# Optimization experiments

Measured on AMD Instinct MI355X. Metric: run time of the kernel, lower is better.

Reference implementation:

```python
import jax, jax.numpy as jnp
import numpy as np

GROUP_SIZE = 16
MIN_SIGMA = 1e-4


def setup_inputs() -> dict:
    key = jax.random.key(0)
    k1, k2, k3 = jax.random.split(key, 3)
    B, N, M, F = 4, 8192, 4096, 64
    return {
        "point_cloud": jax.random.normal(k1, (B, 3, N), dtype=jnp.float32),
        "query_cloud": jax.random.normal(k2, (B, 3, M), dtype=jnp.float32),
        "point_features": jax.random.normal(k3, (B, F, N), dtype=jnp.float32),
        "temperature": jnp.asarray(1.0, dtype=jnp.float32),
    }


def reference(point_cloud, query_cloud, point_features, temperature):
    # point_cloud: (B,3,N), query_cloud: (B,3,M), point_features: (B,F,N)
    k = GROUP_SIZE
    # Pairwise squared distances (B, M, N): ||q||^2 + ||p||^2 - 2 q.p
    q_sq = jnp.sum(query_cloud ** 2, axis=1)              # (B, M)
    p_sq = jnp.sum(point_cloud ** 2, axis=1)              # (B, N)
    qp = jnp.einsum('bdm,bdn->bmn', query_cloud, point_cloud)
    d2 = q_sq[:, :, None] + p_sq[:, None, :] - 2.0 * qp   # (B, M, N)
    # k nearest neighbors per query
    _, idx = jax.lax.top_k(-d2, k)                         # (B, M, k)

    # Gather neighbor coords and features: (B, 3, M, k), (B, F, M, k)
    idx_b = idx[:, None, :, :]                             # (B,1,M,k)
    grouped_points = jnp.take_along_axis(
        point_cloud[:, :, None, :], jnp.broadcast_to(idx_b, (idx.shape[0], 3, idx.shape[1], k)), axis=3)
    grouped_features = jnp.take_along_axis(
        point_features[:, :, None, :],
        jnp.broadcast_to(idx_b, (idx.shape[0], point_features.shape[1], idx.shape[1], k)), axis=3)

    # Soft-projection weights
    sigma = jnp.maximum(temperature ** 2, jnp.asarray(MIN_SIGMA, dtype=temperature.dtype))
    deltas = grouped_points - query_cloud[:, :, :, None]   # (B,3,M,k)
    dist = jnp.sum(deltas ** 2, axis=1, keepdims=True) / sigma  # (B,1,M,k)
    weights = jax.nn.softmax(-dist, axis=3)                # (B,1,M,k)

    projected_points = jnp.sum(grouped_points * weights, axis=3)     # (B,3,M)
    propagated_features = jnp.sum(grouped_features * weights, axis=3)  # (B,F,M)
    return (projected_points, propagated_features)
```

## Files before the change

kernel.cpp:

```cpp
#include <hip/hip_runtime.h>


#define BB 4
#define NN 8192
#define MM 4096
#define FF 64
#define KK 16
#define CHUNK 2048
#define NCHUNK 4
#define QPW 4
#define QPB 32
#define SCAP 54
#define NTHR 1024
#define STG 33

__global__ __launch_bounds__(256) void transpose_feat(const float* __restrict__ pf,
                                                      float* __restrict__ pfT) {
    __shared__ float tile[64][65];
    const int b = blockIdx.y;
    const int n0 = blockIdx.x * 64;
    const int t = threadIdx.x;
    const int n = t & 63, fq = t >> 6;
#pragma unroll
    for (int i = 0; i < 16; ++i) {
        int f = fq * 16 + i;
        tile[f][n] = pf[(size_t)b * FF * NN + (size_t)f * NN + n0 + n];
    }
    __syncthreads();
    const int f2 = t & 63, nq = t >> 6;
#pragma unroll
    for (int i = 0; i < 16; ++i) {
        int nn2 = nq * 16 + i;
        pfT[(size_t)b * NN * FF + (size_t)(n0 + nn2) * FF + f2] = tile[f2][nn2];
    }
}

__device__ __forceinline__ unsigned mapf(float f) {
    unsigned u = __float_as_uint(f);
    return (u & 0x80000000u) ? ~u : (u | 0x80000000u);
}
__device__ __forceinline__ float unmapf(unsigned k) {
    return (k & 0x80000000u) ? __uint_as_float(k ^ 0x80000000u)
                             : __uint_as_float(~k);
}

#define STAGE(C)                                                            \
    do {                                                                    \
        if (t < CHUNK / 4) {                                                \
            int base_ = (C)*CHUNK + t * 4;                                  \
            float4 x4_ = *(const float4*)(pcb + base_);                     \
            float4 y4_ = *(const float4*)(pcb + NN + base_);                \
            float4 z4_ = *(const float4*)(pcb + 2 * NN + base_);            \
            *(float4*)(s_pts + t * 4) = x4_;                                \
            *(float4*)(s_pts + CHUNK + t * 4) = y4_;                        \
            *(float4*)(s_pts + 2 * CHUNK + t * 4) = z4_;                    \
            float4 p4_;                                                     \
            p4_.x = fmaf(x4_.x, x4_.x, fmaf(y4_.x, y4_.x, z4_.x * z4_.x));  \
            p4_.y = fmaf(x4_.y, x4_.y, fmaf(y4_.y, y4_.y, z4_.y * z4_.y));  \
            p4_.z = fmaf(x4_.z, x4_.z, fmaf(y4_.z, y4_.z, z4_.z * z4_.z));  \
            p4_.w = fmaf(x4_.w, x4_.w, fmaf(y4_.w, y4_.w, z4_.w * z4_.w));  \
            *(float4*)(s_pts + 3 * CHUNK + t * 4) = p4_;                    \
        }                                                                   \
    } while (0)

#define VAL(X, Y, Z, PS, Q) \
    fmaf((X), qx2[Q], fmaf((Y), qy2[Q], fmaf((Z), qz2[Q], (PS))))

#define PUSH(WQ, V, I)                                          \
    do {                                                        \
        int pos_ = atomicAdd(&s_cnt[WQ], 1);                    \
        if (pos_ < SCAP) {                                      \
            s_surv[((WQ)*SCAP + pos_) * 2] = (V);               \
            s_surv[((WQ)*SCAP + pos_) * 2 + 1] = __int_as_float(I); \
        }                                                       \
    } while (0)

__global__ __launch_bounds__(NTHR, 8) void soft_proj_kernel(
    const float* __restrict__ pc, const float* __restrict__ qc,
    const float* __restrict__ pf, const float* __restrict__ pfT,
    const float* __restrict__ temp, float* __restrict__ out, int useT) {
    __shared__ __align__(16) float s_pts[4 * CHUNK];
    __shared__ __align__(16) float s_surv[QPB * SCAP * 2];
    __shared__ int s_cnt[QPB];
    __shared__ int s_sel[QPB * KK];
    __shared__ float s_thr[2 * QPB];

    const int bid = blockIdx.x;
    const int b = bid >> 7;
    const int m0 = (bid & 127) * QPB;
    const int t = threadIdx.x;
    const int wave = t >> 6;
    const int lane = t & 63;
    const int pairIdx = wave & 7;
    const int half = wave >> 3;

    const float* pcb = pc + (size_t)b * 3 * NN;
    const float* qcb = qc + (size_t)b * 3 * MM;

    float qx2[QPW], qy2[QPW], qz2[QPW];
#pragma unroll
    for (int q = 0; q < QPW; ++q) {
        int m = m0 + pairIdx * QPW + q;
        qx2[q] = -2.0f * qcb[m];
        qy2[q] = -2.0f * qcb[MM + m];
        qz2[q] = -2.0f * qcb[2 * MM + m];
    }

    float mn[QPW];
#pragma unroll
    for (int q = 0; q < QPW; ++q) mn[q] = 3.0e38f;

    for (int c = 0; c < NCHUNK; ++c) {
        __syncthreads();
        STAGE(c);
        __syncthreads();
        const int ob = half * 1024 + lane * 4;
#pragma unroll
        for (int g = 0; g < 4; ++g) {
            int oo = ob + g * 256;
            float4 x4 = *(const float4*)(s_pts + oo);
            float4 y4 = *(const float4*)(s_pts + CHUNK + oo);
            float4 z4 = *(const float4*)(s_pts + 2 * CHUNK + oo);
            float4 p4 = *(const float4*)(s_pts + 3 * CHUNK + oo);
#pragma unroll
            for (int q = 0; q < QPW; ++q) {
                float v0 = VAL(x4.x, y4.x, z4.x, p4.x, q);
                float v1 = VAL(x4.y, y4.y, z4.y, p4.y, q);
                float v2 = VAL(x4.z, y4.z, z4.z, p4.z, q);
                float v3 = VAL(x4.w, y4.w, z4.w, p4.w, q);
                mn[q] = fminf(mn[q], fminf(fminf(v0, v1), fminf(v2, v3)));
            }
        }
    }

    float thrv[QPW];
#pragma unroll
    for (int q = 0; q < QPW; ++q) {
        unsigned key = mapf(mn[q]);
        unsigned res = 0u;
        for (int bb = 31; bb >= 16; --bb) {
            unsigned cand = res | (1u << bb);
            unsigned long long bal = __ballot(key < cand);
            int c2 = __popcll(bal);
            if (c2 < 8) res = cand;
        }
        thrv[q] = unmapf(res | 0xFFFFu);
    }
    if (lane == 0) {
#pragma unroll
        for (int q = 0; q < QPW; ++q)
            s_thr[half * QPB + pairIdx * QPW + q] = thrv[q];
    }
    if (t < QPB) s_cnt[t] = 0;
    __syncthreads();
#pragma unroll
    for (int q = 0; q < QPW; ++q)
        thrv[q] = fmaxf(s_thr[pairIdx * QPW + q], s_thr[QPB + pairIdx * QPW + q]);

    for (int c = 0; c < NCHUNK; ++c) {
        __syncthreads();
        STAGE(c);
        __syncthreads();
        const int ob = half * 1024 + lane * 4;
#pragma unroll
        for (int g = 0; g < 4; ++g) {
            int oo = ob + g * 256;
            float4 x4 = *(const float4*)(s_pts + oo);
            float4 y4 = *(const float4*)(s_pts + CHUNK + oo);
            float4 z4 = *(const float4*)(s_pts + 2 * CHUNK + oo);
            float4 p4 = *(const float4*)(s_pts + 3 * CHUNK + oo);
            int gi = c * CHUNK + oo;
#pragma unroll
            for (int q = 0; q < QPW; ++q) {
                float v0 = VAL(x4.x, y4.x, z4.x, p4.x, q);
                float v1 = VAL(x4.y, y4.y, z4.y, p4.y, q);
                float v2 = VAL(x4.z, y4.z, z4.z, p4.z, q);
                float v3 = VAL(x4.w, y4.w, z4.w, p4.w, q);
                float m01 = fminf(v0, v1);
                float m23 = fminf(v2, v3);
                if (fminf(m01, m23) <= thrv[q]) {
                    int wqq = pairIdx * QPW + q;
                    if (v0 <= thrv[q]) PUSH(wqq, v0, gi + 0);
                    if (v1 <= thrv[q]) PUSH(wqq, v1, gi + 1);
                    if (v2 <= thrv[q]) PUSH(wqq, v2, gi + 2);
                    if (v3 <= thrv[q]) PUSH(wqq, v3, gi + 3);
                }
            }
        }
    }
    __syncthreads();

#pragma unroll
    for (int qq = 0; qq < 2; ++qq) {
        int wq = wave * 2 + qq;
        int cnt = s_cnt[wq];
        cnt = __builtin_amdgcn_readfirstlane(cnt);
        if (cnt > SCAP) cnt = SCAP;
        bool valid = lane < cnt;
        float mv = 0.f;
        int mi = 0;
        if (valid) {
            mv = s_surv[(wq * SCAP + lane) * 2];
            mi = __float_as_int(s_surv[(wq * SCAP + lane) * 2 + 1]);
        }
        int rank = 0;
        for (int j = 0; j < cnt; ++j) {
            float vj = s_surv[(wq * SCAP + j) * 2];
            int ij = __float_as_int(s_surv[(wq * SCAP + j) * 2 + 1]);
            if (valid && (vj < mv || (vj == mv && ij < mi))) rank++;
        }
        if (valid && rank < KK) s_sel[wq * KK + rank] = mi;
    }
    __syncthreads();

    float* stage = s_surv;
    float tval = temp[0];
    float sigma = fmaxf(tval * tval, 1.0e-4f);
    float inv_sigma = 1.0f / sigma;
    const float* pfTb = pfT + (size_t)b * NN * FF;
    const float* pfb = pf + (size_t)b * FF * NN;

#pragma unroll
    for (int qq = 0; qq < 2; ++qq) {
        int wq = wave * 2 + qq;
        int m = m0 + wq;
        float qxe = qcb[m], qye = qcb[MM + m], qze = qcb[2 * MM + m];
        int ik[KK];
        float dk[KK];
#pragma unroll
        for (int k = 0; k < KK; ++k) {
            int ii = __builtin_amdgcn_readfirstlane(s_sel[wq * KK + k]);
            ik[k] = ii;
            float px = pcb[ii], py = pcb[NN + ii], pz = pcb[2 * NN + ii];
            float dx = px - qxe, dy = py - qye, dz = pz - qze;
            dk[k] = fmaf(dx, dx, fmaf(dy, dy, dz * dz));
        }
        float dmin = dk[0];
#pragma unroll
        for (int k = 1; k < KK; ++k) dmin = fminf(dmin, dk[k]);
        float ssum = 0.f, facc = 0.f, sx = 0.f, sy = 0.f, sz = 0.f;
#pragma unroll
        for (int k = 0; k < KK; ++k) {
            float e = __expf((dmin - dk[k]) * inv_sigma);
            ssum += e;
            float px = pcb[ik[k]], py = pcb[NN + ik[k]], pz = pcb[2 * NN + ik[k]];
            sx = fmaf(e, px, sx);
            sy = fmaf(e, py, sy);
            sz = fmaf(e, pz, sz);
            float fv = useT ? pfTb[(size_t)ik[k] * FF + lane]
                            : pfb[(size_t)lane * NN + ik[k]];
            facc = fmaf(e, fv, facc);
        }
        float rs = 1.0f / ssum;
        stage[lane * STG + wq] = facc * rs;
        if (lane == 0) {
            stage[(64) * STG + wq] = sx * rs;
            stage[(65) * STG + wq] = sy * rs;
            stage[(66) * STG + wq] = sz * rs;
        }
    }
    __syncthreads();

    const size_t featOff = (size_t)BB * 3 * MM;
    for (int j = t; j < 67 * QPB; j += NTHR) {
        int row = j >> 5, col = j & 31;
        float v = stage[row * STG + col];
        int m = m0 + col;
        if (row < 64)
            out[featOff + (size_t)b * FF * MM + (size_t)row * MM + m] = v;
        else
            out[(size_t)b * 3 * MM + (size_t)(row - 64) * MM + m] = v;
    }
}

extern "C" void kernel_launch(void* const* d_in, const int* in_sizes, int n_in,
                              void* d_out, int out_size, void* d_ws, size_t ws_size,
                              hipStream_t stream) {
    (void)in_sizes; (void)n_in; (void)out_size;
    const float* pc = (const float*)d_in[0];
    const float* qc = (const float*)d_in[1];
    const float* pf = (const float*)d_in[2];
    const float* temp = (const float*)d_in[3];
    float* out = (float*)d_out;
    float* pfT = (float*)d_ws;
    const size_t needT = (size_t)BB * NN * FF * sizeof(float);
    int useT = (ws_size >= needT && d_ws != nullptr) ? 1 : 0;

    if (useT) {
        hipLaunchKernelGGL(transpose_feat, dim3(NN / 64, BB), dim3(256), 0, stream,
                           pf, pfT);
    }
    hipLaunchKernelGGL(soft_proj_kernel, dim3((BB * MM) / QPB), dim3(NTHR), 0,
                       stream, pc, qc, pf, pfT, temp, out, useT);
}
```

Measured before the change: 119.5 us.

## Double-buffer point chunks with async global-to-LDS loads and precomputed norms

Point coordinates plus squared norms are precomputed into a 4-plane workspace buffer by the prep kernel. Both scan passes then stream half-size chunks through double-buffered LDS using global_load_lds DMA, so the next chunk loads while the current one is evaluated, and one barrier per chunk replaces two. The min reductions use v_min3 with two independent accumulators. In exchange it needs extra workspace and twice as many chunk iterations.

```diff
diff --git a/kernel.cpp b/kernel.cpp
--- a/kernel.cpp
+++ b/kernel.cpp
@@ -6,20 +6,47 @@
 #define MM 4096
 #define FF 64
 #define KK 16
-#define CHUNK 2048
-#define NCHUNK 4
+#define CHUNK 1024
+#define NCHUNK 8
 #define QPW 4
 #define QPB 32
 #define SCAP 54
 #define NTHR 1024
 #define STG 33
 
-__global__ __launch_bounds__(256) void transpose_feat(const float* __restrict__ pf,
-                                                      float* __restrict__ pfT) {
-    __shared__ float tile[64][65];
+__device__ __forceinline__ void gload_lds16(const float* g, float* l) {
+    __builtin_amdgcn_global_load_lds(
+        (const __attribute__((address_space(1))) void*)g,
+        (__attribute__((address_space(3))) void*)l, 16, 0, 0);
+}
+
+__device__ __forceinline__ float min3f(float a, float b, float c) {
+    float d;
+    asm("v_min3_f32 %0, %1, %2, %3" : "=v"(d) : "v"(a), "v"(b), "v"(c));
+    return d;
+}
+
+__global__ __launch_bounds__(256) void prep_kernel(const float* __restrict__ pf,
+                                                   float* __restrict__ pfT,
+                                                   const float* __restrict__ pc,
+                                                   float* __restrict__ pc4,
+                                                   int doT, int doPS) {
     const int b = blockIdx.y;
     const int n0 = blockIdx.x * 64;
     const int t = threadIdx.x;
+    if (doPS && t < 64) {
+        int n = n0 + t;
+        const float* s = pc + (size_t)b * 3 * NN;
+        float x = s[n], y = s[NN + n], z = s[2 * NN + n];
+        float ps = fmaf(x, x, fmaf(y, y, z * z));
+        float* d = pc4 + (size_t)b * 4 * NN;
+        d[n] = x;
+        d[NN + n] = y;
+        d[2 * NN + n] = z;
+        d[3 * NN + n] = ps;
+    }
+    if (!doT) return;
+    __shared__ float tile[64][65];
     const int n = t & 63, fq = t >> 6;
 #pragma unroll
     for (int i = 0; i < 16; ++i) {
@@ -44,22 +71,28 @@
                              : __uint_as_float(~k);
 }
 
-#define STAGE(C)                                                            \
+#define ISSUE(C, BUF)                                                       \
     do {                                                                    \
-        if (t < CHUNK / 4) {                                                \
+        if (usePS) {                                                        \
+            int pl_ = t >> 8;                                               \
+            int ii_ = (t & 255) * 4;                                        \
+            gload_lds16(pc4b + pl_ * NN + (C)*CHUNK + ii_,                  \
+                        s_pts + (BUF) * (4 * CHUNK) + pl_ * CHUNK + ii_);   \
+        } else if (t < 256) {                                               \
             int base_ = (C)*CHUNK + t * 4;                                  \
             float4 x4_ = *(const float4*)(pcb + base_);                     \
             float4 y4_ = *(const float4*)(pcb + NN + base_);                \
             float4 z4_ = *(const float4*)(pcb + 2 * NN + base_);            \
-            *(float4*)(s_pts + t * 4) = x4_;                                \
-            *(float4*)(s_pts + CHUNK + t * 4) = y4_;                        \
-            *(float4*)(s_pts + 2 * CHUNK + t * 4) = z4_;                    \
+            float* bp_ = s_pts + (BUF) * (4 * CHUNK);                       \
+            *(float4*)(bp_ + t * 4) = x4_;                                  \
+            *(float4*)(bp_ + CHUNK + t * 4) = y4_;                          \
+            *(float4*)(bp_ + 2 * CHUNK + t * 4) = z4_;                      \
             float4 p4_;                                                     \
             p4_.x = fmaf(x4_.x, x4_.x, fmaf(y4_.x, y4_.x, z4_.x * z4_.x));  \
             p4_.y = fmaf(x4_.y, x4_.y, fmaf(y4_.y, y4_.y, z4_.y * z4_.y));  \
             p4_.z = fmaf(x4_.z, x4_.z, fmaf(y4_.z, y4_.z, z4_.z * z4_.z));  \
             p4_.w = fmaf(x4_.w, x4_.w, fmaf(y4_.w, y4_.w, z4_.w * z4_.w));  \
-            *(float4*)(s_pts + 3 * CHUNK + t * 4) = p4_;                    \
+            *(float4*)(bp_ + 3 * CHUNK + t * 4) = p4_;                      \
         }                                                                   \
     } while (0)
 
@@ -78,8 +111,9 @@
 __global__ __launch_bounds__(NTHR, 8) void soft_proj_kernel(
     const float* __restrict__ pc, const float* __restrict__ qc,
     const float* __restrict__ pf, const float* __restrict__ pfT,
-    const float* __restrict__ temp, float* __restrict__ out, int useT) {
-    __shared__ __align__(16) float s_pts[4 * CHUNK];
+    const float* __restrict__ pc4g, const float* __restrict__ temp,
+    float* __restrict__ out, int useT, int usePS) {
+    __shared__ __align__(16) float s_pts[2 * 4 * CHUNK];
     __shared__ __align__(16) float s_surv[QPB * SCAP * 2];
     __shared__ int s_cnt[QPB];
     __shared__ int s_sel[QPB * KK];
@@ -96,6 +130,7 @@
 
     const float* pcb = pc + (size_t)b * 3 * NN;
     const float* qcb = qc + (size_t)b * 3 * MM;
+    const float* pc4b = pc4g + (size_t)b * 4 * NN;
 
     float qx2[QPW], qy2[QPW], qz2[QPW];
 #pragma unroll
@@ -106,37 +141,40 @@
         qz2[q] = -2.0f * qcb[2 * MM + m];
     }
 
-    float mn[QPW];
-#pragma unroll
-    for (int q = 0; q < QPW; ++q) mn[q] = 3.0e38f;
-
+    float mnA[QPW], mnB[QPW];
+#pragma unroll
+    for (int q = 0; q < QPW; ++q) { mnA[q] = 3.0e38f; mnB[q] = 3.0e38f; }
+
+    ISSUE(0, 0);
+    __syncthreads();
     for (int c = 0; c < NCHUNK; ++c) {
-        __syncthreads();
-        STAGE(c);
-        __syncthreads();
-        const int ob = half * 1024 + lane * 4;
-#pragma unroll
-        for (int g = 0; g < 4; ++g) {
+        if (c + 1 < NCHUNK) ISSUE(c + 1, (c + 1) & 1);
+        const float* bp = s_pts + (c & 1) * (4 * CHUNK);
+        const int ob = half * 512 + lane * 4;
+#pragma unroll
+        for (int g = 0; g < 2; ++g) {
             int oo = ob + g * 256;
-            float4 x4 = *(const float4*)(s_pts + oo);
-            float4 y4 = *(const float4*)(s_pts + CHUNK + oo);
-            float4 z4 = *(const float4*)(s_pts + 2 * CHUNK + oo);
-            float4 p4 = *(const float4*)(s_pts + 3 * CHUNK + oo);
+            float4 x4 = *(const float4*)(bp + oo);
+            float4 y4 = *(const float4*)(bp + CHUNK + oo);
+            float4 z4 = *(const float4*)(bp + 2 * CHUNK + oo);
+            float4 p4 = *(const float4*)(bp + 3 * CHUNK + oo);
 #pragma unroll
             for (int q = 0; q < QPW; ++q) {
                 float v0 = VAL(x4.x, y4.x, z4.x, p4.x, q);
                 float v1 = VAL(x4.y, y4.y, z4.y, p4.y, q);
                 float v2 = VAL(x4.z, y4.z, z4.z, p4.z, q);
                 float v3 = VAL(x4.w, y4.w, z4.w, p4.w, q);
-                mn[q] = fminf(mn[q], fminf(fminf(v0, v1), fminf(v2, v3)));
+                mnA[q] = min3f(v0, v1, mnA[q]);
+                mnB[q] = min3f(v2, v3, mnB[q]);
             }
         }
+        __syncthreads();
     }
 
     float thrv[QPW];
 #pragma unroll
     for (int q = 0; q < QPW; ++q) {
-        unsigned key = mapf(mn[q]);
+        unsigned key = mapf(fminf(mnA[q], mnB[q]));
         unsigned res = 0u;
         for (int bb = 31; bb >= 16; --bb) {
             unsigned cand = res | (1u << bb);
@@ -157,18 +195,19 @@
     for (int q = 0; q < QPW; ++q)
         thrv[q] = fmaxf(s_thr[pairIdx * QPW + q], s_thr[QPB + pairIdx * QPW + q]);
 
+    ISSUE(0, 0);
+    __syncthreads();
     for (int c = 0; c < NCHUNK; ++c) {
-        __syncthreads();
-        STAGE(c);
-        __syncthreads();
-        const int ob = half * 1024 + lane * 4;
-#pragma unroll
-        for (int g = 0; g < 4; ++g) {
+        if (c + 1 < NCHUNK) ISSUE(c + 1, (c + 1) & 1);
+        const float* bp = s_pts + (c & 1) * (4 * CHUNK);
+        const int ob = half * 512 + lane * 4;
+#pragma unroll
+        for (int g = 0; g < 2; ++g) {
             int oo = ob + g * 256;
-            float4 x4 = *(const float4*)(s_pts + oo);
-            float4 y4 = *(const float4*)(s_pts + CHUNK + oo);
-            float4 z4 = *(const float4*)(s_pts + 2 * CHUNK + oo);
-            float4 p4 = *(const float4*)(s_pts + 3 * CHUNK + oo);
+            float4 x4 = *(const float4*)(bp + oo);
+            float4 y4 = *(const float4*)(bp + CHUNK + oo);
+            float4 z4 = *(const float4*)(bp + 2 * CHUNK + oo);
+            float4 p4 = *(const float4*)(bp + 3 * CHUNK + oo);
             int gi = c * CHUNK + oo;
 #pragma unroll
             for (int q = 0; q < QPW; ++q) {
@@ -176,9 +215,7 @@
                 float v1 = VAL(x4.y, y4.y, z4.y, p4.y, q);
                 float v2 = VAL(x4.z, y4.z, z4.z, p4.z, q);
                 float v3 = VAL(x4.w, y4.w, z4.w, p4.w, q);
-                float m01 = fminf(v0, v1);
-                float m23 = fminf(v2, v3);
-                if (fminf(m01, m23) <= thrv[q]) {
+                if (fminf(min3f(v0, v1, v2), v3) <= thrv[q]) {
                     int wqq = pairIdx * QPW + q;
                     if (v0 <= thrv[q]) PUSH(wqq, v0, gi + 0);
                     if (v1 <= thrv[q]) PUSH(wqq, v1, gi + 1);
@@ -187,8 +224,8 @@
                 }
             }
         }
-    }
-    __syncthreads();
+        __syncthreads();
+    }
 
 #pragma unroll
     for (int qq = 0; qq < 2; ++qq) {
@@ -284,12 +321,15 @@
     float* out = (float*)d_out;
     float* pfT = (float*)d_ws;
     const size_t needT = (size_t)BB * NN * FF * sizeof(float);
+    const size_t needPS = (size_t)BB * 4 * NN * sizeof(float);
     int useT = (ws_size >= needT && d_ws != nullptr) ? 1 : 0;
-
-    if (useT) {
-        hipLaunchKernelGGL(transpose_feat, dim3(NN / 64, BB), dim3(256), 0, stream,
-                           pf, pfT);
+    int usePS = (ws_size >= needT + needPS && d_ws != nullptr) ? 1 : 0;
+    float* pc4 = (float*)((char*)d_ws + needT);
+
+    if (useT || usePS) {
+        hipLaunchKernelGGL(prep_kernel, dim3(NN / 64, BB), dim3(256), 0, stream,
+                           pf, pfT, pc, pc4, useT, usePS);
     }
     hipLaunchKernelGGL(soft_proj_kernel, dim3((BB * MM) / QPB), dim3(NTHR), 0,
-                       stream, pc, qc, pf, pfT, temp, out, useT);
-}
+                       stream, pc, qc, pf, pfT, pc4, temp, out, useT, usePS);
+}
```

After: 122.5 us. 1.02x slower.
